# Performance work log

Measured on AMD Instinct MI355X. Metric: run time of the kernel, lower is better.

Reference implementation:

```python
import jax, jax.numpy as jnp
import numpy as np

N_NODES = 50000
N_EDGES = 800000
F_IN, HID, N_CLS = 128, 64, 40
KS = 2  # kernel_size, dim=1, open B-spline, degree=1


def spline_conv(x, src, dst, pseudo, W, root, bias, num_nodes, kernel_size):
    """SplineConv (torch_geometric), dim=1, degree=1, open spline, aggr='mean'."""
    K = kernel_size
    v = pseudo[:, 0] * (K - 1)                       # map [0,1] -> [0, K-1]
    k0 = jnp.clip(jnp.floor(v), 0, K - 2)
    frac = v - k0                                    # linear (degree-1) basis
    i0 = k0.astype(jnp.int32)
    i1 = i0 + 1
    E = src.shape[0]
    e = jnp.arange(E)
    # per-edge kernel coefficients c[e,k] = sum_s basis[e,s]*[idx[e,s]==k]
    c = jnp.zeros((E, K), x.dtype).at[e, i0].add(1.0 - frac).at[e, i1].add(frac)
    xj = x[src]                                      # [E, F_in] gather
    # agg[k] = scatter-add over edges of c[e,k]*xj[e] -> [K, N, F_in]
    agg = jnp.stack([
        jax.ops.segment_sum(c[:, k:k + 1] * xj, dst, num_segments=num_nodes)
        for k in range(K)
    ])
    deg = jax.ops.segment_sum(jnp.ones((E,), x.dtype), dst, num_segments=num_nodes)
    msg = jnp.einsum('kni,kio->no', agg, W) / jnp.maximum(deg, 1.0)[:, None]
    return msg + x @ root + bias


def setup_inputs() -> dict:
    key = jax.random.key(0)
    ks = jax.random.split(key, 9)
    def glorot(k, shape):
        fan_in, fan_out = shape[-2], shape[-1]
        lim = (6.0 / (fan_in + fan_out)) ** 0.5
        return jax.random.uniform(k, shape, jnp.float32, -lim, lim)
    return {
        'x': jax.random.normal(ks[0], (N_NODES, F_IN), jnp.float32),
        'edge_index': jax.random.randint(ks[1], (2, N_EDGES), 0, N_NODES, jnp.int32),
        'edge_attr': jax.random.uniform(ks[2], (N_EDGES, 1), jnp.float32),
        'W1': glorot(ks[3], (KS, F_IN, HID)),
        'root1': glorot(ks[4], (F_IN, HID)),
        'bias1': jnp.zeros((HID,), jnp.float32),
        'W2': glorot(ks[5], (KS, HID, N_CLS)),
        'root2': glorot(ks[6], (HID, N_CLS)),
        'bias2': jnp.zeros((N_CLS,), jnp.float32),
    }


def reference(x, edge_index, edge_attr, W1, root1, bias1, W2, root2, bias2):
    src, dst = edge_index[0], edge_index[1]
    # eval mode: dropout is identity
    h = spline_conv(x, src, dst, edge_attr, W1, root1, bias1, N_NODES, KS)
    h = jax.nn.elu(h)
    out = spline_conv(h, src, dst, edge_attr, W2, root2, bias2, N_NODES, KS)
    return out
```

## Files before the change

### kernel.cpp

```cpp
#include <hip/hip_runtime.h>
#include <math.h>

#define N_NODES 50000
#define N_EDGES 800000
#define F_IN    128
#define HID     64
#define N_CLS   40

#define M1 (3 * HID)
#define M2P 128

#define RANGE_SZ 6250
#define PERM_SLICES 128
#define PERM_CHUNK (N_EDGES / PERM_SLICES)
#define EST 64

#define NW 32768

using sh8 = __attribute__((ext_vector_type(8))) short;
using floatx4 = __attribute__((ext_vector_type(4))) float;

__device__ inline unsigned short f2bf(float f) {
    union { float f; unsigned int u; } c{f};
    unsigned int r = (c.u + 0x7FFF + ((c.u >> 16) & 1)) >> 16;
    return (unsigned short)r;
}
__device__ inline float bf2f(unsigned int u) {
    union { unsigned int u; float f; } c;
    c.u = u << 16;
    return c.f;
}

__global__ void concat_w(const float* __restrict__ W1, const float* __restrict__ root1,
                         const float* __restrict__ W2, const float* __restrict__ root2,
                         unsigned short* __restrict__ WT1, unsigned short* __restrict__ WT2,
                         int* __restrict__ cnt) {
    int i = blockIdx.x * blockDim.x + threadIdx.x;
    if (i < M1 * F_IN) {
        int c = i / F_IN, k = i % F_IN;
        float val;
        if (c < HID)            val = W1[k * HID + c];
        else if (c < 2 * HID)   val = W1[F_IN * HID + k * HID + (c - HID)];
        else                    val = root1[k * HID + (c - 2 * HID)];
        WT1[i] = f2bf(val);
    } else if (i < NW) {
        int ii = i - M1 * F_IN;
        int c = ii / HID, k = ii % HID;
        float val;
        if (c < N_CLS)            val = W2[k * N_CLS + c];
        else if (c < 2 * N_CLS)   val = W2[HID * N_CLS + k * N_CLS + (c - N_CLS)];
        else if (c < 3 * N_CLS)   val = root2[k * N_CLS + (c - 2 * N_CLS)];
        else                      val = 0.0f;
        WT2[ii] = f2bf(val);
    } else {
        int ii = i - NW;
        if (ii < N_NODES) cnt[ii] = 0;
    }
}

template <int KD, bool AF32, int SPLIT, int PW, int ROOTW, int MT>
__device__ __forceinline__ void gemm_body(int bid, const void* __restrict__ Aptr,
                                          const unsigned short* __restrict__ Bt,
                                          unsigned short* __restrict__ Csp,
                                          float* __restrict__ Croot, int Crows) {
    constexpr int KP = KD + 8;
    __shared__ unsigned short As[64 * KP];
    __shared__ unsigned short Bs[64 * KP];

    int tid = threadIdx.x;
    int row0 = bid * 64;

    if (AF32) {
        const float* A = (const float*)Aptr;
        for (int c = tid; c < 64 * (KD / 4); c += 256) {
            int r = c / (KD / 4), q = c % (KD / 4);
            int gr = row0 + r;
            float4 v = make_float4(0.f, 0.f, 0.f, 0.f);
            if (gr < Crows) v = *(const float4*)(A + (size_t)gr * KD + q * 4);
            union { unsigned short s[4]; uint2 u; } pk;
            pk.s[0] = f2bf(v.x); pk.s[1] = f2bf(v.y);
            pk.s[2] = f2bf(v.z); pk.s[3] = f2bf(v.w);
            *(uint2*)&As[r * KP + q * 4] = pk.u;
        }
    } else {
        const unsigned short* A = (const unsigned short*)Aptr;
        for (int c = tid; c < 64 * (KD / 8); c += 256) {
            int r = c / (KD / 8), q = c % (KD / 8);
            int gr = row0 + r;
            sh8 v = {};
            if (gr < Crows) v = *(const sh8*)(A + (size_t)gr * KD + q * 8);
            *(sh8*)&As[r * KP + q * 8] = v;
        }
    }

    int wv = tid >> 6, lane = tid & 63;
    int lrow = lane & 15, lq = lane >> 4;

    for (int mt = 0; mt < MT; ++mt) {
        int c0 = mt * 64;
        __syncthreads();
        for (int c = tid; c < 64 * (KD / 8); c += 256) {
            int r = c / (KD / 8), q = c % (KD / 8);
            *(sh8*)&Bs[r * KP + q * 8] = *(const sh8*)(Bt + (size_t)(c0 + r) * KD + q * 8);
        }
        __syncthreads();

        floatx4 acc[4] = {{0.f,0.f,0.f,0.f},{0.f,0.f,0.f,0.f},{0.f,0.f,0.f,0.f},{0.f,0.f,0.f,0.f}};
#pragma unroll
        for (int kt = 0; kt < KD / 32; ++kt) {
            int kb = kt * 32 + lq * 8;
            sh8 a0 = *(const sh8*)&As[(wv * 16 + lrow) * KP + kb];
#pragma unroll
            for (int cf = 0; cf < 4; ++cf) {
                sh8 b = *(const sh8*)&Bs[(cf * 16 + lrow) * KP + kb];
                acc[cf] = __builtin_amdgcn_mfma_f32_16x16x32_bf16(a0, b, acc[cf], 0, 0, 0);
            }
        }

#pragma unroll
        for (int r = 0; r < 4; ++r) {
            int gr = row0 + wv * 16 + lq * 4 + r;
            if (gr >= Crows) continue;
#pragma unroll
            for (int cf = 0; cf < 4; ++cf) {
                int gc = c0 + cf * 16 + lrow;
                float val = acc[cf][r];
                if (gc < SPLIT) {
                    int pi = (gc < PW) ? gc * 2 : (gc - PW) * 2 + 1;
                    Csp[(size_t)gr * SPLIT + pi] = f2bf(val);
                } else if (gc < SPLIT + ROOTW) {
                    Croot[(size_t)gr * ROOTW + (gc - SPLIT)] = val;
                }
            }
        }
    }
}

__device__ __forceinline__ void permute_body(int b, const int* __restrict__ src,
                                             const int* __restrict__ dst,
                                             const float* __restrict__ attr,
                                             int* __restrict__ cnt,
                                             unsigned int* __restrict__ edata) {
    int range = b & 7;
    int slice = b >> 3;
    int lo = range * RANGE_SZ;
    int e0 = slice * PERM_CHUNK;
    int e1 = e0 + PERM_CHUNK;
    for (int e = e0 + (int)threadIdx.x; e < e1; e += 256) {
        int d = dst[e];
        if ((unsigned)(d - lo) < (unsigned)RANGE_SZ) {
            int pos = atomicAdd(&cnt[d], 1);
            if (pos < EST) {
                unsigned int q = (unsigned int)(attr[e] * 65535.0f + 0.5f);
                edata[d * EST + pos] = (unsigned int)src[e] | (q << 16);
            }
        }
    }
}

__global__ __launch_bounds__(256) void gemm1_permute(const float* __restrict__ x,
                                                     const unsigned short* __restrict__ WT1,
                                                     unsigned short* __restrict__ Ysp,
                                                     float* __restrict__ Yroot,
                                                     const int* __restrict__ src,
                                                     const int* __restrict__ dst,
                                                     const float* __restrict__ attr,
                                                     int* __restrict__ cnt,
                                                     unsigned int* __restrict__ edata,
                                                     int gemmBlocks) {
    if ((int)blockIdx.x < gemmBlocks) {
        gemm_body<128, true, 128, 64, 64, 3>(blockIdx.x, (const void*)x, WT1, Ysp, Yroot, N_NODES);
    } else {
        permute_body(blockIdx.x - gemmBlocks, src, dst, attr, cnt, edata);
    }
}

template <int KD, bool AF32, int SPLIT, int PW, int ROOTW, int MT>
__global__ __launch_bounds__(256) void gemm_mfma(const void* __restrict__ Aptr,
                                                 const unsigned short* __restrict__ Bt,
                                                 unsigned short* __restrict__ Csp,
                                                 float* __restrict__ Croot,
                                                 int Crows) {
    gemm_body<KD, AF32, SPLIT, PW, ROOTW, MT>(blockIdx.x, Aptr, Bt, Csp, Croot, Crows);
}

__global__ __launch_bounds__(256) void gather1(const unsigned short* __restrict__ Ysp,
                                               const float* __restrict__ Yroot,
                                               const int* __restrict__ cnt,
                                               const unsigned int* __restrict__ edata,
                                               const float* __restrict__ bias1,
                                               unsigned short* __restrict__ h) {
    int wave = (blockIdx.x * blockDim.x + threadIdx.x) >> 6;
    int lane = threadIdx.x & 63;
    if (wave >= N_NODES) return;
    int deg = cnt[wave];
    deg = deg > EST ? EST : deg;
    const unsigned int* eb = edata + (size_t)wave * EST;
    const float qs = 1.0f / 65535.0f;
    float acc = 0.0f;
    if (deg <= 16) {
        unsigned int e[16], p[16];
#pragma unroll
        for (int t = 0; t < 16; ++t) e[t] = eb[t];
#pragma unroll
        for (int t = 0; t < 16; ++t) {
            int idx = (t < deg) ? (int)(e[t] & 0xffffu) : 0;
            p[t] = *(const unsigned int*)(Ysp + (size_t)idx * 128 + lane * 2);
        }
#pragma unroll
        for (int t = 0; t < 16; ++t) {
            float m = (t < deg) ? 1.0f : 0.0f;
            float v = (float)(e[t] >> 16) * qs;
            acc += m * ((1.0f - v) * bf2f(p[t] & 0xffffu) + v * bf2f(p[t] >> 16));
        }
    } else {
        unsigned int e[32], p[32];
#pragma unroll
        for (int t = 0; t < 32; ++t) e[t] = eb[t];
#pragma unroll
        for (int t = 0; t < 32; ++t) {
            int idx = (t < deg) ? (int)(e[t] & 0xffffu) : 0;
            p[t] = *(const unsigned int*)(Ysp + (size_t)idx * 128 + lane * 2);
        }
#pragma unroll
        for (int t = 0; t < 32; ++t) {
            float m = (t < deg) ? 1.0f : 0.0f;
            float v = (float)(e[t] >> 16) * qs;
            acc += m * ((1.0f - v) * bf2f(p[t] & 0xffffu) + v * bf2f(p[t] >> 16));
        }
        if (deg > 32) {
            for (int j = 32; j < deg; j += 8) {
                unsigned int e2[8], p2[8];
#pragma unroll
                for (int t = 0; t < 8; ++t) e2[t] = eb[j + t];
#pragma unroll
                for (int t = 0; t < 8; ++t) {
                    int idx = (j + t < deg) ? (int)(e2[t] & 0xffffu) : 0;
                    p2[t] = *(const unsigned int*)(Ysp + (size_t)idx * 128 + lane * 2);
                }
#pragma unroll
                for (int t = 0; t < 8; ++t) {
                    float m = (j + t < deg) ? 1.0f : 0.0f;
                    float v = (float)(e2[t] >> 16) * qs;
                    acc += m * ((1.0f - v) * bf2f(p2[t] & 0xffffu) + v * bf2f(p2[t] >> 16));
                }
            }
        }
    }
    float dg = (float)deg;
    dg = dg > 1.0f ? dg : 1.0f;
    float m = acc / dg + Yroot[(size_t)wave * HID + lane] + bias1[lane];
    m = m > 0.0f ? m : expm1f(m);
    h[(size_t)wave * HID + lane] = f2bf(m);
}

__global__ __launch_bounds__(256) void gather2(const unsigned short* __restrict__ Zsp,
                                               const float* __restrict__ Zroot,
                                               const int* __restrict__ cnt,
                                               const unsigned int* __restrict__ edata,
                                               const float* __restrict__ bias2,
                                               float* __restrict__ out) {
    int wave = (blockIdx.x * blockDim.x + threadIdx.x) >> 6;
    int lane = threadIdx.x & 63;
    if (wave >= N_NODES) return;
    if (lane >= N_CLS) return;
    int deg = cnt[wave];
    deg = deg > EST ? EST : deg;
    const unsigned int* eb = edata + (size_t)wave * EST;
    const float qs = 1.0f / 65535.0f;
    float acc = 0.0f;
    if (deg <= 16) {
        unsigned int e[16], p[16];
#pragma unroll
        for (int t = 0; t < 16; ++t) e[t] = eb[t];
#pragma unroll
        for (int t = 0; t < 16; ++t) {
            int idx = (t < deg) ? (int)(e[t] & 0xffffu) : 0;
            p[t] = *(const unsigned int*)(Zsp + (size_t)idx * 80 + lane * 2);
        }
#pragma unroll
        for (int t = 0; t < 16; ++t) {
            float m = (t < deg) ? 1.0f : 0.0f;
            float v = (float)(e[t] >> 16) * qs;
            acc += m * ((1.0f - v) * bf2f(p[t] & 0xffffu) + v * bf2f(p[t] >> 16));
        }
    } else {
        unsigned int e[32], p[32];
#pragma unroll
        for (int t = 0; t < 32; ++t) e[t] = eb[t];
#pragma unroll
        for (int t = 0; t < 32; ++t) {
            int idx = (t < deg) ? (int)(e[t] & 0xffffu) : 0;
            p[t] = *(const unsigned int*)(Zsp + (size_t)idx * 80 + lane * 2);
        }
#pragma unroll
        for (int t = 0; t < 32; ++t) {
            float m = (t < deg) ? 1.0f : 0.0f;
            float v = (float)(e[t] >> 16) * qs;
            acc += m * ((1.0f - v) * bf2f(p[t] & 0xffffu) + v * bf2f(p[t] >> 16));
        }
        if (deg > 32) {
            for (int j = 32; j < deg; j += 8) {
                unsigned int e2[8], p2[8];
#pragma unroll
                for (int t = 0; t < 8; ++t) e2[t] = eb[j + t];
#pragma unroll
                for (int t = 0; t < 8; ++t) {
                    int idx = (j + t < deg) ? (int)(e2[t] & 0xffffu) : 0;
                    p2[t] = *(const unsigned int*)(Zsp + (size_t)idx * 80 + lane * 2);
                }
#pragma unroll
                for (int t = 0; t < 8; ++t) {
                    float m = (j + t < deg) ? 1.0f : 0.0f;
                    float v = (float)(e2[t] >> 16) * qs;
                    acc += m * ((1.0f - v) * bf2f(p2[t] & 0xffffu) + v * bf2f(p2[t] >> 16));
                }
            }
        }
    }
    float dg = (float)deg;
    dg = dg > 1.0f ? dg : 1.0f;
    out[(size_t)wave * N_CLS + lane] =
        acc / dg + Zroot[(size_t)wave * N_CLS + lane] + bias2[lane];
}

extern "C" void kernel_launch(void* const* d_in, const int* in_sizes, int n_in,
                              void* d_out, int out_size, void* d_ws, size_t ws_size,
                              hipStream_t stream) {
    const float* x     = (const float*)d_in[0];
    const int*   eidx  = (const int*)d_in[1];
    const float* eattr = (const float*)d_in[2];
    const float* W1    = (const float*)d_in[3];
    const float* root1 = (const float*)d_in[4];
    const float* bias1 = (const float*)d_in[5];
    const float* W2    = (const float*)d_in[6];
    const float* root2 = (const float*)d_in[7];
    const float* bias2 = (const float*)d_in[8];
    float* out = (float*)d_out;

    const int* src = eidx;
    const int* dst = eidx + N_EDGES;

    char* base = (char*)d_ws;
    unsigned short* Ysp   = (unsigned short*)base;
    float*          Yroot = (float*)(base + 12800000);
    unsigned short* hb    = (unsigned short*)(base + 25600000);
    unsigned short* WT1   = (unsigned short*)(base + 32000000);
    unsigned short* WT2   = (unsigned short*)(base + 32049152);
    unsigned int*   edata = (unsigned int*)(base + 32065536);
    int*            cnt   = (int*)(base + 44865536);
    unsigned short* Zsp   = Ysp;
    float*          Zroot = Yroot;

    const int GB = (N_NODES + 63) / 64;

    hipLaunchKernelGGL(concat_w, dim3((NW + N_NODES + 255) / 256), dim3(256), 0, stream,
                       W1, root1, W2, root2, WT1, WT2, cnt);

    hipLaunchKernelGGL(gemm1_permute, dim3(GB + 8 * PERM_SLICES), dim3(256), 0, stream,
                       x, WT1, Ysp, Yroot, src, dst, eattr, cnt, edata, GB);
    hipLaunchKernelGGL(gather1, dim3((N_NODES * 64 + 255) / 256), dim3(256), 0, stream,
                       Ysp, Yroot, cnt, edata, bias1, hb);

    hipLaunchKernelGGL((gemm_mfma<64, false, 80, 40, 40, 2>),
                       dim3(GB), dim3(256), 0, stream,
                       (const void*)hb, WT2, Zsp, Zroot, N_NODES);
    hipLaunchKernelGGL(gather2, dim3((N_NODES * 64 + 255) / 256), dim3(256), 0, stream,
                       Zsp, Zroot, cnt, edata, bias2, out);
}
```

Before: 204.8 us.

## Fuse layer-two GEMM into the first gather kernel via shared-memory weights

Removes the separate MFMA GEMM for layer two and the bf16 hidden buffer. Each gather1z block now stages the 64x128 bf16 W2/root2 matrix in shared memory and computes the node's 120 outputs with scalar FMAs after the ELU. It writes Zsp in the interleaved spline layout and Zroot in fp32. This saves a kernel launch and the h round trip. In exchange, every block reloads 16KB of weights into LDS and the matmul runs on scalar ALUs instead of MFMA. WT2 is now laid out k-major so lanes read consecutive columns.

```diff
diff --git a/kernel.cpp b/kernel.cpp
--- a/kernel.cpp
+++ b/kernel.cpp
@@ -45,7 +45,7 @@
         WT1[i] = f2bf(val);
     } else if (i < NW) {
         int ii = i - M1 * F_IN;
-        int c = ii / HID, k = ii % HID;
+        int k = ii >> 7, c = ii & 127;
         float val;
         if (c < N_CLS)            val = W2[k * N_CLS + c];
         else if (c < 2 * N_CLS)   val = W2[HID * N_CLS + k * N_CLS + (c - N_CLS)];
@@ -175,27 +175,32 @@
     }
 }
 
-template <int KD, bool AF32, int SPLIT, int PW, int ROOTW, int MT>
-__global__ __launch_bounds__(256) void gemm_mfma(const void* __restrict__ Aptr,
-                                                 const unsigned short* __restrict__ Bt,
-                                                 unsigned short* __restrict__ Csp,
-                                                 float* __restrict__ Croot,
-                                                 int Crows) {
-    gemm_body<KD, AF32, SPLIT, PW, ROOTW, MT>(blockIdx.x, Aptr, Bt, Csp, Croot, Crows);
-}
-
-__global__ __launch_bounds__(256) void gather1(const unsigned short* __restrict__ Ysp,
-                                               const float* __restrict__ Yroot,
-                                               const int* __restrict__ cnt,
-                                               const unsigned int* __restrict__ edata,
-                                               const float* __restrict__ bias1,
-                                               unsigned short* __restrict__ h) {
-    int wave = (blockIdx.x * blockDim.x + threadIdx.x) >> 6;
-    int lane = threadIdx.x & 63;
-    if (wave >= N_NODES) return;
-    int deg = cnt[wave];
+__global__ __launch_bounds__(256) void gather1z(const unsigned short* __restrict__ Ysp,
+                                                const float* __restrict__ Yroot,
+                                                const int* __restrict__ cnt,
+                                                const unsigned int* __restrict__ edata,
+                                                const float* __restrict__ bias1,
+                                                const unsigned short* __restrict__ WT2,
+                                                unsigned short* __restrict__ Zsp,
+                                                float* __restrict__ Zroot) {
+    __shared__ unsigned short w2s[64 * 128];
+    __shared__ float hs[4 * 64];
+
+    int tid = threadIdx.x;
+    {
+        const uint4* s4 = (const uint4*)WT2;
+        uint4* d4 = (uint4*)w2s;
+        for (int i = tid; i < (64 * 128) / 8; i += 256) d4[i] = s4[i];
+    }
+    __syncthreads();
+
+    int wv = tid >> 6, lane = tid & 63;
+    int node = blockIdx.x * 4 + wv;
+    if (node >= N_NODES) return;
+
+    int deg = cnt[node];
     deg = deg > EST ? EST : deg;
-    const unsigned int* eb = edata + (size_t)wave * EST;
+    const unsigned int* eb = edata + (size_t)node * EST;
     const float qs = 1.0f / 65535.0f;
     float acc = 0.0f;
     if (deg <= 16) {
@@ -249,9 +254,30 @@
     }
     float dg = (float)deg;
     dg = dg > 1.0f ? dg : 1.0f;
-    float m = acc / dg + Yroot[(size_t)wave * HID + lane] + bias1[lane];
+    float m = acc / dg + Yroot[(size_t)node * HID + lane] + bias1[lane];
     m = m > 0.0f ? m : expm1f(m);
-    h[(size_t)wave * HID + lane] = f2bf(m);
+
+    hs[wv * 64 + lane] = m;
+
+    float z0 = 0.0f, z1 = 0.0f;
+#pragma unroll 16
+    for (int k = 0; k < 64; ++k) {
+        float hk = hs[wv * 64 + k];
+        z0 += hk * bf2f(w2s[k * 128 + lane]);
+        z1 += hk * bf2f(w2s[k * 128 + 64 + lane]);
+    }
+
+    {
+        int pi = (lane < N_CLS) ? lane * 2 : (lane - N_CLS) * 2 + 1;
+        Zsp[(size_t)node * 80 + pi] = f2bf(z0);
+    }
+    int c1 = lane + 64;
+    if (c1 < 80) {
+        int pi = (c1 - N_CLS) * 2 + 1;
+        Zsp[(size_t)node * 80 + pi] = f2bf(z1);
+    } else if (c1 < 120) {
+        Zroot[(size_t)node * N_CLS + (c1 - 80)] = z1;
+    }
 }
 
 __global__ __launch_bounds__(256) void gather2(const unsigned short* __restrict__ Zsp,
@@ -344,13 +370,12 @@
     char* base = (char*)d_ws;
     unsigned short* Ysp   = (unsigned short*)base;
     float*          Yroot = (float*)(base + 12800000);
-    unsigned short* hb    = (unsigned short*)(base + 25600000);
     unsigned short* WT1   = (unsigned short*)(base + 32000000);
     unsigned short* WT2   = (unsigned short*)(base + 32049152);
     unsigned int*   edata = (unsigned int*)(base + 32065536);
     int*            cnt   = (int*)(base + 44865536);
-    unsigned short* Zsp   = Ysp;
-    float*          Zroot = Yroot;
+    unsigned short* Zsp   = (unsigned short*)(base + 45065536);
+    float*          Zroot = (float*)(base + 53065536);
 
     const int GB = (N_NODES + 63) / 64;
 
@@ -359,12 +384,10 @@
 
     hipLaunchKernelGGL(gemm1_permute, dim3(GB + 8 * PERM_SLICES), dim3(256), 0, stream,
                        x, WT1, Ysp, Yroot, src, dst, eattr, cnt, edata, GB);
-    hipLaunchKernelGGL(gather1, dim3((N_NODES * 64 + 255) / 256), dim3(256), 0, stream,
-                       Ysp, Yroot, cnt, edata, bias1, hb);
-
-    hipLaunchKernelGGL((gemm_mfma<64, false, 80, 40, 40, 2>),
-                       dim3(GB), dim3(256), 0, stream,
-                       (const void*)hb, WT2, Zsp, Zroot, N_NODES);
+
+    hipLaunchKernelGGL(gather1z, dim3((N_NODES + 3) / 4), dim3(256), 0, stream,
+                       Ysp, Yroot, cnt, edata, bias1, WT2, Zsp, Zroot);
+
     hipLaunchKernelGGL(gather2, dim3((N_NODES * 64 + 255) / 256), dim3(256), 0, stream,
                        Zsp, Zroot, cnt, edata, bias2, out);
 }
```

Result: slower. 213.0 us (+4.0%).
